# Optimization experiments

Hardware: AMD Instinct MI355X
Metric: run time of the kernel (lower is better)

Reference implementation:

```python
import jax, jax.numpy as jnp
import numpy as np

N = 50000
E = 600000
IN_DIM, FEAT_DIM, HID_DIM, OUT_DIM = 256, 128, 128, 64


def _glorot(key, shape):
    fan_in, fan_out = shape[0], shape[1]
    lim = jnp.sqrt(6.0 / (fan_in + fan_out))
    return jax.random.uniform(key, shape, jnp.float32, -lim, lim)


def setup_inputs() -> dict:
    key = jax.random.key(0)
    ks = jax.random.split(key, 10)
    x = jax.random.normal(ks[0], (N, IN_DIM), jnp.float32)
    edge_index = jax.random.randint(ks[1], (2, E), 0, N, jnp.int64)
    return {
        "x": x,
        "edge_index": edge_index,
        # linear_pre: input_dim -> feature_dim
        "W_pre": _glorot(ks[2], (IN_DIM, FEAT_DIM)),
        "b_pre": jnp.zeros((FEAT_DIM,), jnp.float32),
        # conv_first (SAGEConv feature_dim -> hidden_dim): lin_l (neighbors, bias), lin_r (root, no bias)
        "Wl1": _glorot(ks[3], (FEAT_DIM, HID_DIM)),
        "bl1": jnp.zeros((HID_DIM,), jnp.float32),
        "Wr1": _glorot(ks[4], (FEAT_DIM, HID_DIM)),
        # conv_out (SAGEConv hidden_dim -> output_dim)
        "Wl2": _glorot(ks[5], (HID_DIM, OUT_DIM)),
        "bl2": jnp.zeros((OUT_DIM,), jnp.float32),
        "Wr2": _glorot(ks[6], (HID_DIM, OUT_DIM)),
    }


def _sage_conv(x, src, dst, deg_inv, Wl, bl, Wr):
    # mean aggregation of source features at destination nodes
    msgs = x[src]                                            # [E, d]
    aggr = jax.ops.segment_sum(msgs, dst, num_segments=N)    # [N, d]
    aggr = aggr * deg_inv[:, None]
    return aggr @ Wl + bl + x @ Wr


def reference(x, edge_index, W_pre, b_pre, Wl1, bl1, Wr1, Wl2, bl2, Wr2):
    src, dst = edge_index[0], edge_index[1]
    deg = jax.ops.segment_sum(jnp.ones((E,), jnp.float32), dst, num_segments=N)
    deg_inv = jnp.where(deg > 0, 1.0 / jnp.maximum(deg, 1.0), 0.0)

    h = x @ W_pre + b_pre                                    # linear_pre
    h = _sage_conv(h, src, dst, deg_inv, Wl1, bl1, Wr1)      # conv_first
    h = jax.nn.relu(h)
    # dropout: identity in eval mode
    h = _sage_conv(h, src, dst, deg_inv, Wl2, bl2, Wr2)      # conv_out
    norm = jnp.linalg.norm(h, axis=-1, keepdims=True)
    return h / jnp.maximum(norm, 1e-12)                      # F.normalize p=2
```

## Files before the change

kernel.cpp:

```cpp
#include <hip/hip_runtime.h>


#define NN   50000
#define EE   600000
#define NBLK 49
#define NRG64 782

typedef __attribute__((ext_vector_type(8))) _Float16 h8v;
typedef __attribute__((ext_vector_type(4))) _Float16 h4v;
typedef __attribute__((ext_vector_type(2))) _Float16 h2v;
typedef __attribute__((ext_vector_type(8))) short short8v;
typedef __attribute__((ext_vector_type(4))) float f32x4;

__device__ inline h8v h8zero() {
    return __builtin_bit_cast(h8v, (short8v){0,0,0,0,0,0,0,0});
}


__global__ __launch_bounds__(256) void k_count(const int* __restrict__ ei,
                                               int* __restrict__ counts) {
    int e = blockIdx.x * 256 + threadIdx.x;
    if (e < EE) atomicAdd(&counts[ei[EE + e]], 1);
}

__global__ __launch_bounds__(256) void k_scan_a(const int* __restrict__ counts,
                                                int* __restrict__ bsums) {
    int b = blockIdx.x, t = threadIdx.x;
    int idx = b * 1024 + t * 4;
    int s = 0;
#pragma unroll
    for (int j = 0; j < 4; ++j)
        if (idx + j < NN) s += counts[idx + j];
#pragma unroll
    for (int off = 32; off > 0; off >>= 1) s += __shfl_down(s, off);
    __shared__ int ls[4];
    if ((t & 63) == 0) ls[t >> 6] = s;
    __syncthreads();
    if (t == 0) bsums[b] = ls[0] + ls[1] + ls[2] + ls[3];
}

__global__ void k_scan_b(int* __restrict__ bsums) {
    int t = threadIdx.x;
    int v = (t < NBLK) ? bsums[t] : 0;
    int orig = v;
#pragma unroll
    for (int off = 1; off < 64; off <<= 1) {
        int u = __shfl_up(v, off);
        if (t >= off) v += u;
    }
    if (t < NBLK) bsums[t] = v - orig;
}

__global__ __launch_bounds__(256) void k_scan_c(const int* __restrict__ counts,
                                                const int* __restrict__ bsums,
                                                int* __restrict__ rowp) {
    int b = blockIdx.x, t = threadIdx.x;
    int lane = t & 63, wave = t >> 6;
    int idx = b * 1024 + t * 4;
    int c[4], s = 0;
#pragma unroll
    for (int j = 0; j < 4; ++j) {
        c[j] = (idx + j < NN) ? counts[idx + j] : 0;
        s += c[j];
    }
    int sv = s;
#pragma unroll
    for (int off = 1; off < 64; off <<= 1) {
        int u = __shfl_up(sv, off);
        if (lane >= off) sv += u;
    }
    __shared__ int lsum[4];
    if (lane == 63) lsum[wave] = sv;
    __syncthreads();
    int woff = 0;
    for (int wv = 0; wv < wave; ++wv) woff += lsum[wv];
    int base = bsums[b] + woff + (sv - s);
#pragma unroll
    for (int j = 0; j < 4; ++j) {
        if (idx + j < NN) { rowp[idx + j] = base; base += c[j]; }
    }
}

__global__ __launch_bounds__(256) void k_scatter(const int* __restrict__ ei,
                                                 const int* __restrict__ rowp,
                                                 int* __restrict__ cursor,
                                                 int* __restrict__ col) {
    int e = blockIdx.x * 256 + threadIdx.x;
    if (e < EE) {
        int d = ei[EE + e];
        int p = atomicAdd(&cursor[d], 1);
        col[rowp[d] + p] = ei[e];
    }
}


__global__ __launch_bounds__(256) void k_cvt(const float* __restrict__ in,
                                             _Float16* __restrict__ outp, int n4) {
    int i = blockIdx.x * 256 + threadIdx.x;
    if (i >= n4) return;
    float4 v = ((const float4*)in)[i];
    h4v o;
    o[0] = (_Float16)v.x; o[1] = (_Float16)v.y;
    o[2] = (_Float16)v.z; o[3] = (_Float16)v.w;
    ((h4v*)outp)[i] = o;
}


__global__ __launch_bounds__(256) void k_prep(const float* __restrict__ Wpre,
                                              const float* __restrict__ bpre,
                                              const float* __restrict__ Wl1,
                                              const float* __restrict__ Wr1,
                                              const float* __restrict__ Wl2,
                                              const float* __restrict__ Wr2,
                                              _Float16* __restrict__ WAH,
                                              _Float16* __restrict__ WAL,
                                              _Float16* __restrict__ WBH,
                                              _Float16* __restrict__ WBL,
                                              float* __restrict__ bA,
                                              float* __restrict__ bB,
                                              _Float16* __restrict__ W2lH,
                                              _Float16* __restrict__ W2lL,
                                              _Float16* __restrict__ W2rH,
                                              _Float16* __restrict__ W2rL) {
    int idx = blockIdx.x * 256 + threadIdx.x;
    if (idx < 65792) {
        int which = idx / (257 * 128);
        int rem = idx - which * 257 * 128;
        int i = rem >> 7, j = rem & 127;
        const float* W = which ? Wr1 : Wl1;
        float s = 0.f;
        if (i < 256) {
#pragma unroll 4
            for (int k = 0; k < 128; ++k) s += Wpre[i * 128 + k] * W[k * 128 + j];
            _Float16 h = (_Float16)s;
            _Float16 l = (_Float16)(s - (float)h);
            if (which) { WBH[j * 256 + i] = h; WBL[j * 256 + i] = l; }
            else       { WAH[j * 256 + i] = h; WAL[j * 256 + i] = l; }
        } else {
#pragma unroll 4
            for (int k = 0; k < 128; ++k) s += bpre[k] * W[k * 128 + j];
            if (which) bB[j] = s; else bA[j] = s;
        }
    } else {
        int idx2 = idx - 65792;
        int which = idx2 >> 13;
        int rem = idx2 & 8191;
        int k = rem >> 6, m = rem & 63;
        float w = (which ? Wr2 : Wl2)[rem];
        _Float16 h = (_Float16)w;
        _Float16 l = (_Float16)(w - (float)h);
        if (which) { W2rH[m * 128 + k] = h; W2rL[m * 128 + k] = l; }
        else       { W2lH[m * 128 + k] = h; W2lL[m * 128 + k] = l; }
    }
}


__global__ __launch_bounds__(256) void k_gemm_fused(
        const _Float16* __restrict__ xh,
        const _Float16* __restrict__ WAH, const _Float16* __restrict__ WAL,
        const _Float16* __restrict__ WBH, const _Float16* __restrict__ WBL,
        const float* __restrict__ bA, const float* __restrict__ bB,
        _Float16* __restrict__ t1, _Float16* __restrict__ r1) {
    const int wave = threadIdx.x >> 6, lane = threadIdx.x & 63;
    const int r = lane & 15, kb = lane >> 4;
    const int s = ((blockIdx.x & 3) << 2) + wave;
    const int sel = s >> 3;
    const int col = ((s & 7) << 4) + r;
    const _Float16* __restrict__ WH = sel ? WBH : WAH;
    const _Float16* __restrict__ WL = sel ? WBL : WAL;
    _Float16* __restrict__ dst = sel ? r1 : t1;
    const float bias = (sel ? bB : bA)[col];
    const int row0 = (blockIdx.x >> 2) << 6;

    f32x4 acc[4];
#pragma unroll
    for (int a = 0; a < 4; ++a) acc[a] = (f32x4){0.f, 0.f, 0.f, 0.f};

#pragma unroll
    for (int k = 0; k < 8; ++k) {
        size_t woff = (size_t)col * 256 + k * 32 + kb * 8;
        h8v wh = *(const h8v*)&WH[woff];
        h8v wl = *(const h8v*)&WL[woff];
        h8v a[4];
#pragma unroll
        for (int rt = 0; rt < 4; ++rt) {
            int rr = row0 + rt * 16;
            a[rt] = (rr < NN)
                ? *(const h8v*)&xh[(size_t)(rr + r) * 256 + k * 32 + kb * 8]
                : h8zero();
        }
#pragma unroll
        for (int rt = 0; rt < 4; ++rt) {
            acc[rt] = __builtin_amdgcn_mfma_f32_16x16x32_f16(a[rt], wh, acc[rt], 0, 0, 0);
            acc[rt] = __builtin_amdgcn_mfma_f32_16x16x32_f16(a[rt], wl, acc[rt], 0, 0, 0);
        }
    }
#pragma unroll
    for (int rt = 0; rt < 4; ++rt) {
        int rr = row0 + rt * 16;
        if (rr >= NN) continue;
        int rbase = rr + kb * 4;
#pragma unroll
        for (int j = 0; j < 4; ++j)
            dst[(size_t)(rbase + j) * 128 + col] = (_Float16)(acc[rt][j] + bias);
    }
}


__global__ __launch_bounds__(256) void k_gemm_dual2(
        const _Float16* __restrict__ A,
        const _Float16* __restrict__ W1H, const _Float16* __restrict__ W1L,
        const _Float16* __restrict__ W2H, const _Float16* __restrict__ W2L,
        _Float16* __restrict__ T, _Float16* __restrict__ R) {
    const int wave = threadIdx.x >> 6, lane = threadIdx.x & 63;
    const int r = lane & 15, kb = lane >> 4;
    const int s = ((blockIdx.x & 1) << 2) + wave;
    const int sel = s >> 2;
    const int col = ((s & 3) << 4) + r;
    const _Float16* __restrict__ WH = sel ? W2H : W1H;
    const _Float16* __restrict__ WL = sel ? W2L : W1L;
    _Float16* __restrict__ dst = sel ? R : T;
    const int row0 = (blockIdx.x >> 1) << 6;

    f32x4 acc[4];
#pragma unroll
    for (int a = 0; a < 4; ++a) acc[a] = (f32x4){0.f, 0.f, 0.f, 0.f};

#pragma unroll
    for (int k = 0; k < 4; ++k) {
        size_t woff = (size_t)col * 128 + k * 32 + kb * 8;
        h8v wh = *(const h8v*)&WH[woff];
        h8v wl = *(const h8v*)&WL[woff];
        h8v a[4];
#pragma unroll
        for (int rt = 0; rt < 4; ++rt) {
            int rr = row0 + rt * 16;
            a[rt] = (rr < NN)
                ? *(const h8v*)&A[(size_t)(rr + r) * 128 + k * 32 + kb * 8]
                : h8zero();
        }
#pragma unroll
        for (int rt = 0; rt < 4; ++rt) {
            acc[rt] = __builtin_amdgcn_mfma_f32_16x16x32_f16(a[rt], wh, acc[rt], 0, 0, 0);
            acc[rt] = __builtin_amdgcn_mfma_f32_16x16x32_f16(a[rt], wl, acc[rt], 0, 0, 0);
        }
    }
#pragma unroll
    for (int rt = 0; rt < 4; ++rt) {
        int rr = row0 + rt * 16;
        if (rr >= NN) continue;
        int rbase = rr + kb * 4;
#pragma unroll
        for (int j = 0; j < 4; ++j)
            dst[(size_t)(rbase + j) * 64 + col] = (_Float16)acc[rt][j];
    }
}


__global__ __launch_bounds__(256) void k_aggr1(const _Float16* __restrict__ t1,
                                               const _Float16* __restrict__ r1,
                                               const int* __restrict__ rowp,
                                               const int* __restrict__ counts,
                                               const int* __restrict__ col,
                                               const float* __restrict__ bl1,
                                               _Float16* __restrict__ h1) {
    int node = blockIdx.x * 4 + (threadIdx.x >> 6);
    int lane = threadIdx.x & 63;
    if (node >= NN) return;
    int half = lane >> 5, sl = lane & 31;
    int e0 = rowp[node], cnt = counts[node];
    float a0 = 0.f, a1 = 0.f, a2 = 0.f, a3 = 0.f;
    const h4v* T = (const h4v*)t1;
    for (int base = 0; base < cnt; base += 64) {
        int m = cnt - base; if (m > 64) m = 64;
        int myS = (base + lane < cnt) ? col[e0 + base + lane] : 0;
        int i = 0;
        for (; i + 8 <= m; i += 8) {
            int s0 = __shfl(myS, i + 0 + half), s1 = __shfl(myS, i + 2 + half);
            int s2 = __shfl(myS, i + 4 + half), s3 = __shfl(myS, i + 6 + half);
            h4v v0 = T[(size_t)s0 * 32 + sl], v1 = T[(size_t)s1 * 32 + sl];
            h4v v2 = T[(size_t)s2 * 32 + sl], v3 = T[(size_t)s3 * 32 + sl];
            a0 += (float)v0[0] + (float)v1[0] + (float)v2[0] + (float)v3[0];
            a1 += (float)v0[1] + (float)v1[1] + (float)v2[1] + (float)v3[1];
            a2 += (float)v0[2] + (float)v1[2] + (float)v2[2] + (float)v3[2];
            a3 += (float)v0[3] + (float)v1[3] + (float)v2[3] + (float)v3[3];
        }
        for (; i < m; i += 2) {
            if (i + half < m) {
                int s = __shfl(myS, i + half);
                h4v v = T[(size_t)s * 32 + sl];
                a0 += (float)v[0]; a1 += (float)v[1];
                a2 += (float)v[2]; a3 += (float)v[3];
            }
        }
    }
    a0 += __shfl_xor(a0, 32); a1 += __shfl_xor(a1, 32);
    a2 += __shfl_xor(a2, 32); a3 += __shfl_xor(a3, 32);
    float di = (cnt > 0) ? 1.0f / (float)cnt : 0.0f;
    h4v rr = ((const h4v*)r1)[(size_t)node * 32 + sl];
    float4 bb = ((const float4*)bl1)[sl];
    if (half == 0) {
        h4v h;
        h[0] = (_Float16)fmaxf(fmaf(a0, di, bb.x + (float)rr[0]), 0.0f);
        h[1] = (_Float16)fmaxf(fmaf(a1, di, bb.y + (float)rr[1]), 0.0f);
        h[2] = (_Float16)fmaxf(fmaf(a2, di, bb.z + (float)rr[2]), 0.0f);
        h[3] = (_Float16)fmaxf(fmaf(a3, di, bb.w + (float)rr[3]), 0.0f);
        ((h4v*)h1)[(size_t)node * 32 + sl] = h;
    }
}


__global__ __launch_bounds__(256) void k_aggr2(const _Float16* __restrict__ t2,
                                               const _Float16* __restrict__ r2,
                                               const int* __restrict__ rowp,
                                               const int* __restrict__ counts,
                                               const int* __restrict__ col,
                                               const float* __restrict__ bl2,
                                               float* __restrict__ out) {
    int node = blockIdx.x * 4 + (threadIdx.x >> 6);
    int lane = threadIdx.x & 63;
    if (node >= NN) return;
    int half = lane >> 5, sl = lane & 31;
    int e0 = rowp[node], cnt = counts[node];
    float ax = 0.f, ay = 0.f;
    const h2v* T = (const h2v*)t2;
    for (int base = 0; base < cnt; base += 64) {
        int m = cnt - base; if (m > 64) m = 64;
        int myS = (base + lane < cnt) ? col[e0 + base + lane] : 0;
        int i = 0;
        for (; i + 8 <= m; i += 8) {
            int s0 = __shfl(myS, i + 0 + half), s1 = __shfl(myS, i + 2 + half);
            int s2 = __shfl(myS, i + 4 + half), s3 = __shfl(myS, i + 6 + half);
            h2v v0 = T[(size_t)s0 * 32 + sl], v1 = T[(size_t)s1 * 32 + sl];
            h2v v2 = T[(size_t)s2 * 32 + sl], v3 = T[(size_t)s3 * 32 + sl];
            ax += (float)v0[0] + (float)v1[0] + (float)v2[0] + (float)v3[0];
            ay += (float)v0[1] + (float)v1[1] + (float)v2[1] + (float)v3[1];
        }
        for (; i < m; i += 2) {
            if (i + half < m) {
                int s = __shfl(myS, i + half);
                h2v v = T[(size_t)s * 32 + sl];
                ax += (float)v[0]; ay += (float)v[1];
            }
        }
    }
    ax += __shfl_xor(ax, 32);
    ay += __shfl_xor(ay, 32);
    float di = (cnt > 0) ? 1.0f / (float)cnt : 0.0f;
    h2v rr = ((const h2v*)r2)[(size_t)node * 32 + sl];
    float2 bb = ((const float2*)bl2)[sl];
    float v0 = fmaf(ax, di, bb.x + (float)rr[0]);
    float v1 = fmaf(ay, di, bb.y + (float)rr[1]);
    float ss = v0 * v0 + v1 * v1;
#pragma unroll
    for (int off = 16; off > 0; off >>= 1) ss += __shfl_xor(ss, off);
    float inv = 1.0f / fmaxf(sqrtf(ss), 1e-12f);
    if (half == 0)
        ((float2*)out)[(size_t)node * 32 + sl] = make_float2(v0 * inv, v1 * inv);
}


extern "C" void kernel_launch(void* const* d_in, const int* in_sizes, int n_in,
                              void* d_out, int out_size, void* d_ws, size_t ws_size,
                              hipStream_t stream) {
    const float* x    = (const float*)d_in[0];
    const int*   ei   = (const int*)d_in[1];
    const float* Wpre = (const float*)d_in[2];
    const float* bpre = (const float*)d_in[3];
    const float* Wl1  = (const float*)d_in[4];
    const float* bl1  = (const float*)d_in[5];
    const float* Wr1  = (const float*)d_in[6];
    const float* Wl2  = (const float*)d_in[7];
    const float* bl2  = (const float*)d_in[8];
    const float* Wr2  = (const float*)d_in[9];
    float* out = (float*)d_out;

    char* w = (char*)d_ws;
    int* counts = (int*)w;  w += (size_t)NN * 4;
    int* cursor = (int*)w;  w += (size_t)NN * 4;
    int* rowp   = (int*)w;  w += (size_t)NN * 4;
    int* bsums  = (int*)w;  w += 256;
    int* col    = (int*)w;  w += (size_t)EE * 4;
    _Float16* WAH  = (_Float16*)w; w += (size_t)256 * 128 * 2;
    _Float16* WAL  = (_Float16*)w; w += (size_t)256 * 128 * 2;
    _Float16* WBH  = (_Float16*)w; w += (size_t)256 * 128 * 2;
    _Float16* WBL  = (_Float16*)w; w += (size_t)256 * 128 * 2;
    float*    bA   = (float*)w;    w += 128 * 4;
    float*    bB   = (float*)w;    w += 128 * 4;
    _Float16* W2lH = (_Float16*)w; w += (size_t)128 * 64 * 2;
    _Float16* W2lL = (_Float16*)w; w += (size_t)128 * 64 * 2;
    _Float16* W2rH = (_Float16*)w; w += (size_t)128 * 64 * 2;
    _Float16* W2rL = (_Float16*)w; w += (size_t)128 * 64 * 2;
    _Float16* xh   = (_Float16*)w; w += (size_t)NN * 256 * 2;
    _Float16* t1   = (_Float16*)w; w += (size_t)NN * 128 * 2;
    _Float16* r1   = (_Float16*)w; w += (size_t)NN * 128 * 2;
    _Float16* h1   = (_Float16*)w; w += (size_t)NN * 128 * 2;
    _Float16* t2   = (_Float16*)w; w += (size_t)NN * 64 * 2;
    _Float16* r2   = (_Float16*)w; w += (size_t)NN * 64 * 2;

    hipMemsetAsync(counts, 0, (size_t)NN * 8, stream);

    dim3 b256(256);
    dim3 gE((EE + 255) / 256);
    k_count<<<gE, b256, 0, stream>>>(ei, counts);
    k_scan_a<<<dim3(NBLK), b256, 0, stream>>>(counts, bsums);
    k_scan_b<<<dim3(1), dim3(64), 0, stream>>>(bsums);
    k_scan_c<<<dim3(NBLK), b256, 0, stream>>>(counts, bsums, rowp);
    k_scatter<<<gE, b256, 0, stream>>>(ei, rowp, cursor, col);

    k_cvt<<<dim3(NN * 256 / 4 / 256), b256, 0, stream>>>(x, xh, NN * 256 / 4);
    k_prep<<<dim3(321), b256, 0, stream>>>(Wpre, bpre, Wl1, Wr1, Wl2, Wr2,
                                           WAH, WAL, WBH, WBL, bA, bB,
                                           W2lH, W2lL, W2rH, W2rL);

    k_gemm_fused<<<dim3(NRG64 * 4), b256, 0, stream>>>(xh, WAH, WAL, WBH, WBL,
                                                       bA, bB, t1, r1);
    k_aggr1<<<dim3((NN + 3) / 4), b256, 0, stream>>>(t1, r1, rowp, counts, col, bl1, h1);
    k_gemm_dual2<<<dim3(NRG64 * 2), b256, 0, stream>>>(h1, W2lH, W2lL, W2rH, W2rL, t2, r2);
    k_aggr2<<<dim3((NN + 3) / 4), b256, 0, stream>>>(t2, r2, rowp, counts, col, bl2, out);
}
```

Before: 338.8 us.

## Stage A tile in swizzled LDS and compute all output columns per block

```diff
diff --git a/kernel.cpp b/kernel.cpp
--- a/kernel.cpp
+++ b/kernel.cpp
@@ -161,48 +161,71 @@
         const _Float16* __restrict__ WBH, const _Float16* __restrict__ WBL,
         const float* __restrict__ bA, const float* __restrict__ bB,
         _Float16* __restrict__ t1, _Float16* __restrict__ r1) {
-    const int wave = threadIdx.x >> 6, lane = threadIdx.x & 63;
+    __shared__ char As[64 * 512];
+    const int t = threadIdx.x;
+    const int wave = t >> 6, lane = t & 63;
     const int r = lane & 15, kb = lane >> 4;
-    const int s = ((blockIdx.x & 3) << 2) + wave;
-    const int sel = s >> 3;
-    const int col = ((s & 7) << 4) + r;
+    const int row0 = blockIdx.x << 6;
+
+#pragma unroll
+    for (int j = 0; j < 8; ++j) {
+        int id = t + (j << 8);
+        int row = id >> 5, c16 = id & 31;
+        int gr = row0 + row;
+        h8v v = (gr < NN) ? *(const h8v*)&xh[(size_t)gr * 256 + (c16 << 3)]
+                          : h8zero();
+        *(h8v*)&As[row * 512 + (((c16 << 4)) ^ ((row & 7) << 4))] = v;
+    }
+    __syncthreads();
+
+    const int sel = wave >> 1;
     const _Float16* __restrict__ WH = sel ? WBH : WAH;
     const _Float16* __restrict__ WL = sel ? WBL : WAL;
     _Float16* __restrict__ dst = sel ? r1 : t1;
-    const float bias = (sel ? bB : bA)[col];
-    const int row0 = (blockIdx.x >> 2) << 6;
-
-    f32x4 acc[4];
-#pragma unroll
-    for (int a = 0; a < 4; ++a) acc[a] = (f32x4){0.f, 0.f, 0.f, 0.f};
+    const float* __restrict__ bias = sel ? bB : bA;
+    const int colbase = (wave & 1) << 6;
+
+    f32x4 acc[4][4];
+#pragma unroll
+    for (int sl = 0; sl < 4; ++sl)
+#pragma unroll
+        for (int rt = 0; rt < 4; ++rt) acc[sl][rt] = (f32x4){0.f, 0.f, 0.f, 0.f};
 
 #pragma unroll
     for (int k = 0; k < 8; ++k) {
-        size_t woff = (size_t)col * 256 + k * 32 + kb * 8;
-        h8v wh = *(const h8v*)&WH[woff];
-        h8v wl = *(const h8v*)&WL[woff];
         h8v a[4];
 #pragma unroll
         for (int rt = 0; rt < 4; ++rt) {
-            int rr = row0 + rt * 16;
-            a[rt] = (rr < NN)
-                ? *(const h8v*)&xh[(size_t)(rr + r) * 256 + k * 32 + kb * 8]
-                : h8zero();
-        }
+            int row = (rt << 4) + r;
+            a[rt] = *(const h8v*)&As[row * 512 +
+                                     (((k << 6) + (kb << 4)) ^ ((row & 7) << 4))];
+        }
+#pragma unroll
+        for (int sl = 0; sl < 4; ++sl) {
+            size_t woff = (size_t)(colbase + (sl << 4) + r) * 256 + (k << 5) + (kb << 3);
+            h8v wh = *(const h8v*)&WH[woff];
+            h8v wl = *(const h8v*)&WL[woff];
+#pragma unroll
+            for (int rt = 0; rt < 4; ++rt) {
+                acc[sl][rt] = __builtin_amdgcn_mfma_f32_16x16x32_f16(a[rt], wh, acc[sl][rt], 0, 0, 0);
+                acc[sl][rt] = __builtin_amdgcn_mfma_f32_16x16x32_f16(a[rt], wl, acc[sl][rt], 0, 0, 0);
+            }
+        }
+    }
+#pragma unroll
+    for (int sl = 0; sl < 4; ++sl) {
+        int col = colbase + (sl << 4) + r;
+        float b = bias[col];
 #pragma unroll
         for (int rt = 0; rt < 4; ++rt) {
-            acc[rt] = __builtin_amdgcn_mfma_f32_16x16x32_f16(a[rt], wh, acc[rt], 0, 0, 0);
-            acc[rt] = __builtin_amdgcn_mfma_f32_16x16x32_f16(a[rt], wl, acc[rt], 0, 0, 0);
-        }
-    }
-#pragma unroll
-    for (int rt = 0; rt < 4; ++rt) {
-        int rr = row0 + rt * 16;
-        if (rr >= NN) continue;
-        int rbase = rr + kb * 4;
-#pragma unroll
-        for (int j = 0; j < 4; ++j)
-            dst[(size_t)(rbase + j) * 128 + col] = (_Float16)(acc[rt][j] + bias);
+            int rbase = row0 + (rt << 4) + (kb << 2);
+#pragma unroll
+            for (int j = 0; j < 4; ++j) {
+                int rr = rbase + j;
+                if (rr < NN)
+                    dst[(size_t)rr * 128 + col] = (_Float16)(acc[sl][rt][j] + b);
+            }
+        }
     }
 }
 
@@ -212,47 +235,69 @@
         const _Float16* __restrict__ W1H, const _Float16* __restrict__ W1L,
         const _Float16* __restrict__ W2H, const _Float16* __restrict__ W2L,
         _Float16* __restrict__ T, _Float16* __restrict__ R) {
-    const int wave = threadIdx.x >> 6, lane = threadIdx.x & 63;
+    __shared__ char As[64 * 256];
+    const int t = threadIdx.x;
+    const int wave = t >> 6, lane = t & 63;
     const int r = lane & 15, kb = lane >> 4;
-    const int s = ((blockIdx.x & 1) << 2) + wave;
-    const int sel = s >> 2;
-    const int col = ((s & 3) << 4) + r;
+    const int row0 = blockIdx.x << 6;
+
+#pragma unroll
+    for (int j = 0; j < 4; ++j) {
+        int id = t + (j << 8);
+        int row = id >> 4, c16 = id & 15;
+        int gr = row0 + row;
+        h8v v = (gr < NN) ? *(const h8v*)&A[(size_t)gr * 128 + (c16 << 3)]
+                          : h8zero();
+        *(h8v*)&As[row * 256 + (((c16 << 4)) ^ ((row & 7) << 4))] = v;
+    }
+    __syncthreads();
+
+    const int sel = wave >> 1;
     const _Float16* __restrict__ WH = sel ? W2H : W1H;
     const _Float16* __restrict__ WL = sel ? W2L : W1L;
     _Float16* __restrict__ dst = sel ? R : T;
-    const int row0 = (blockIdx.x >> 1) << 6;
-
-    f32x4 acc[4];
-#pragma unroll
-    for (int a = 0; a < 4; ++a) acc[a] = (f32x4){0.f, 0.f, 0.f, 0.f};
+    const int colbase = (wave & 1) << 5;
+
+    f32x4 acc[2][4];
+#pragma unroll
+    for (int sl = 0; sl < 2; ++sl)
+#pragma unroll
+        for (int rt = 0; rt < 4; ++rt) acc[sl][rt] = (f32x4){0.f, 0.f, 0.f, 0.f};
 
 #pragma unroll
     for (int k = 0; k < 4; ++k) {
-        size_t woff = (size_t)col * 128 + k * 32 + kb * 8;
-        h8v wh = *(const h8v*)&WH[woff];
-        h8v wl = *(const h8v*)&WL[woff];
         h8v a[4];
 #pragma unroll
         for (int rt = 0; rt < 4; ++rt) {
-            int rr = row0 + rt * 16;
-            a[rt] = (rr < NN)
-                ? *(const h8v*)&A[(size_t)(rr + r) * 128 + k * 32 + kb * 8]
-                : h8zero();
-        }
+            int row = (rt << 4) + r;
+            a[rt] = *(const h8v*)&As[row * 256 +
+                                     (((k << 6) + (kb << 4)) ^ ((row & 7) << 4))];
+        }
+#pragma unroll
+        for (int sl = 0; sl < 2; ++sl) {
+            size_t woff = (size_t)(colbase + (sl << 4) + r) * 128 + (k << 5) + (kb << 3);
+            h8v wh = *(const h8v*)&WH[woff];
+            h8v wl = *(const h8v*)&WL[woff];
+#pragma unroll
+            for (int rt = 0; rt < 4; ++rt) {
+                acc[sl][rt] = __builtin_amdgcn_mfma_f32_16x16x32_f16(a[rt], wh, acc[sl][rt], 0, 0, 0);
+                acc[sl][rt] = __builtin_amdgcn_mfma_f32_16x16x32_f16(a[rt], wl, acc[sl][rt], 0, 0, 0);
+            }
+        }
+    }
+#pragma unroll
+    for (int sl = 0; sl < 2; ++sl) {
+        int col = colbase + (sl << 4) + r;
 #pragma unroll
         for (int rt = 0; rt < 4; ++rt) {
-            acc[rt] = __builtin_amdgcn_mfma_f32_16x16x32_f16(a[rt], wh, acc[rt], 0, 0, 0);
-            acc[rt] = __builtin_amdgcn_mfma_f32_16x16x32_f16(a[rt], wl, acc[rt], 0, 0, 0);
-        }
-    }
-#pragma unroll
-    for (int rt = 0; rt < 4; ++rt) {
-        int rr = row0 + rt * 16;
-        if (rr >= NN) continue;
-        int rbase = rr + kb * 4;
-#pragma unroll
-        for (int j = 0; j < 4; ++j)
-            dst[(size_t)(rbase + j) * 64 + col] = (_Float16)acc[rt][j];
+            int rbase = row0 + (rt << 4) + (kb << 2);
+#pragma unroll
+            for (int j = 0; j < 4; ++j) {
+                int rr = rbase + j;
+                if (rr < NN)
+                    dst[(size_t)rr * 64 + col] = (_Float16)acc[sl][rt][j];
+            }
+        }
     }
 }
 
@@ -413,9 +458,9 @@
                                            WAH, WAL, WBH, WBL, bA, bB,
                                            W2lH, W2lL, W2rH, W2rL);
 
-    k_gemm_fused<<<dim3(NRG64 * 4), b256, 0, stream>>>(xh, WAH, WAL, WBH, WBL,
-                                                       bA, bB, t1, r1);
+    k_gemm_fused<<<dim3(NRG64), b256, 0, stream>>>(xh, WAH, WAL, WBH, WBL,
+                                                   bA, bB, t1, r1);
     k_aggr1<<<dim3((NN + 3) / 4), b256, 0, stream>>>(t1, r1, rowp, counts, col, bl1, h1);
-    k_gemm_dual2<<<dim3(NRG64 * 2), b256, 0, stream>>>(h1, W2lH, W2lL, W2rH, W2rL, t2, r2);
+    k_gemm_dual2<<<dim3(NRG64), b256, 0, stream>>>(h1, W2lH, W2lL, W2rH, W2rL, t2, r2);
     k_aggr2<<<dim3((NN + 3) / 4), b256, 0, stream>>>(t2, r2, rowp, counts, col, bl2, out);
 }
```

Result: faster. 312.3 us (-7.8%).
